# Performance work log

Measured on AMD Instinct MI355X. Metric: run time of the kernel, lower is better.

Reference implementation:

```python
import jax, jax.numpy as jnp
import numpy as np

B, T, V, R = 512, 24, 32000, 32
# Scale keeps both the selected chain (factor ~ sqrt(R)*c per step) and the
# vocab-marginalized chain (factor ~ sqrt(V*R)*c per step) inside fp32 range.
CORE_SCALE = (R * np.sqrt(V)) ** -0.5


def setup_inputs() -> dict:
    key = jax.random.key(0)
    k1, k2, k3, k4 = jax.random.split(key, 4)
    y = jax.random.randint(k1, (B, T), 0, V)                      # (B, T) token ids
    alpha = jax.random.normal(k2, (1, R), dtype=jnp.float32)      # left boundary
    beta = jax.random.normal(k3, (1, R), dtype=jnp.float32)       # right boundary
    core = jax.random.normal(k4, (1, R, V, R), dtype=jnp.float32) * CORE_SCALE
    return {"y": y, "alpha": alpha, "beta": beta, "core": core}


def _mps_fwd(alpha, beta, core, y):
    a = alpha[0]                                   # (R,)
    b = beta[0]                                    # (R,)
    cores = jnp.transpose(core[0], (1, 0, 2))      # (V, R, R): per-token transfer matrices
    bsz, seq = y.shape

    # --- unnormalized p(y): chain of selected R x R matrices (marginalize_mask = 0) ---
    sel = jnp.moveaxis(cores[y], 1, 0)             # (T, B, R, R) gathered transfer matrices
    init = jnp.broadcast_to(a, (bsz, R))           # (B, R)

    def step(state, M):                            # state: (B, R), M: (B, R, R)
        return jnp.einsum('br,brs->bs', state, M), None

    state, _ = jax.lax.scan(step, init, sel)
    p_tilde = state @ b                            # (B,)

    # --- normalization: every position marginalized over vocab (free pos-0 leg also summed) ---
    m = cores.sum(axis=0)                          # (R, R) marginalized transfer matrix

    def zstep(v, _):                               # v: (R,)
        return v @ m, None

    vz, _ = jax.lax.scan(zstep, a, None, length=seq)
    z = (vz @ b) * bsz                             # z_one is identical per row; .sum() over batch

    return jnp.concatenate([p_tilde, z[None]])     # (B + 1,): [p_tilde..., z]


def reference(y, alpha, beta, core):
    return _mps_fwd(alpha, beta, core, y)
```

## Files before the change

### kernel.cpp

```cpp
#include <hip/hip_runtime.h>

#define RNK 32
#define VOC 32000
#define BSZ 512
#define SEQ 24

#define CHAIN_BLOCKS 512
#define RED_CHUNKS 125
#define REDUCE_BLOCKS (32 * RED_CHUNKS)
#define DEPTH 6

typedef const __attribute__((address_space(1))) void* as1_cvp;
typedef __attribute__((address_space(3))) void* as3_vp;

__device__ __forceinline__ void issue_matrix_load(const float* src_tok,
                                                  float* lds_base, int lane) {
    const int r  = lane >> 3;
    const int c0 = (lane & 7) * 4;
    #pragma unroll
    for (int j = 0; j < 4; ++j) {
        const float* src = src_tok + (size_t)(j * 8 + r) * ((size_t)VOC * RNK) + c0;
        __builtin_amdgcn_global_load_lds((as1_cvp)src, (as3_vp)(lds_base + j * 256), 16, 0, 0);
    }
}

__global__ __launch_bounds__(64) void fused_kernel(const float* __restrict__ core,
                                                   const int* __restrict__ y,
                                                   const float* __restrict__ alpha,
                                                   const float* __restrict__ beta,
                                                   float* __restrict__ out,
                                                   float* __restrict__ gm) {
    __shared__ float mbuf[DEPTH * 1024];

    const int tid = threadIdx.x;

    if (blockIdx.x < CHAIN_BLOCKS) {
        const int lane = tid;
        const int s    = lane & 31;
        const int half = lane >> 5;
        const int row  = blockIdx.x;

        int   ytok  = (lane < SEQ) ? y[row * SEQ + lane] : 0;
        float state = alpha[s];
        float betav = beta[s];

        asm volatile("s_waitcnt vmcnt(0)" ::: "memory");

        #pragma unroll
        for (int pt = 0; pt < DEPTH; ++pt) {
            const int tok = __shfl(ytok, pt, 64);
            issue_matrix_load(core + (size_t)tok * RNK, mbuf + pt * 1024, lane);
        }

        #pragma unroll
        for (int t = 0; t < SEQ; ++t) {
            if      (t <= SEQ - 6) asm volatile("s_waitcnt vmcnt(20)" ::: "memory");
            else if (t == SEQ - 5) asm volatile("s_waitcnt vmcnt(16)" ::: "memory");
            else if (t == SEQ - 4) asm volatile("s_waitcnt vmcnt(12)" ::: "memory");
            else if (t == SEQ - 3) asm volatile("s_waitcnt vmcnt(8)"  ::: "memory");
            else if (t == SEQ - 2) asm volatile("s_waitcnt vmcnt(4)"  ::: "memory");
            else                   asm volatile("s_waitcnt vmcnt(0)"  ::: "memory");
            __builtin_amdgcn_sched_barrier(0);

            if (t + DEPTH < SEQ) {
                const int tok = __shfl(ytok, t + DEPTH, 64);
                issue_matrix_load(core + (size_t)tok * RNK,
                                  mbuf + ((t + DEPTH) % DEPTH) * 1024, lane);
            }

            const float* M = mbuf + (t % DEPTH) * 1024;
            float a0 = 0.f, a1 = 0.f, a2 = 0.f, a3 = 0.f;
            #pragma unroll
            for (int i = 0; i < 16; i += 4) {
                a0 = fmaf(__shfl(state, half * 16 + i + 0, 64), M[(half * 16 + i + 0) * 32 + s], a0);
                a1 = fmaf(__shfl(state, half * 16 + i + 1, 64), M[(half * 16 + i + 1) * 32 + s], a1);
                a2 = fmaf(__shfl(state, half * 16 + i + 2, 64), M[(half * 16 + i + 2) * 32 + s], a2);
                a3 = fmaf(__shfl(state, half * 16 + i + 3, 64), M[(half * 16 + i + 3) * 32 + s], a3);
            }
            const float acc = (a0 + a1) + (a2 + a3);
            state = acc + __shfl_xor(acc, 32, 64);
        }

        float p = state * betav;
        #pragma unroll
        for (int m = 16; m >= 1; m >>= 1) p += __shfl_xor(p, m, 64);
        if (lane == 0) out[row] = p;
    } else {
        const int bid   = blockIdx.x - CHAIN_BLOCKS;
        const int r     = bid & 31;
        const int chunk = bid >> 5;

        const float4* slab = (const float4*)(core + (size_t)r * VOC * RNK);
        const int base = chunk * 2048 + tid;

        float a0 = 0.f, a1 = 0.f, a2 = 0.f, a3 = 0.f;
        #pragma unroll
        for (int i = 0; i < 32; ++i) {
            float4 v = slab[base + i * 64];
            a0 += v.x; a1 += v.y; a2 += v.z; a3 += v.w;
        }

        #pragma unroll
        for (int mask = 8; mask <= 32; mask <<= 1) {
            a0 += __shfl_xor(a0, mask, 64);
            a1 += __shfl_xor(a1, mask, 64);
            a2 += __shfl_xor(a2, mask, 64);
            a3 += __shfl_xor(a3, mask, 64);
        }
        if (tid < 8) {
            const int s0 = tid * 4;
            atomicAdd(&gm[r * RNK + s0 + 0], a0);
            atomicAdd(&gm[r * RNK + s0 + 1], a1);
            atomicAdd(&gm[r * RNK + s0 + 2], a2);
            atomicAdd(&gm[r * RNK + s0 + 3], a3);
        }
    }
}

__global__ void zchain_kernel(const float* __restrict__ gm,
                              const float* __restrict__ alpha,
                              const float* __restrict__ beta,
                              float* __restrict__ out) {
    const int lane = threadIdx.x & 63;
    const int s    = lane & 31;
    const int half = lane >> 5;

    float col[16];
    #pragma unroll
    for (int i = 0; i < 16; ++i) col[i] = gm[(half * 16 + i) * RNK + s];

    float v = alpha[s];
    #pragma unroll
    for (int t = 0; t < SEQ; ++t) {
        float a0 = 0.f, a1 = 0.f, a2 = 0.f, a3 = 0.f;
        #pragma unroll
        for (int i = 0; i < 16; i += 4) {
            a0 = fmaf(__shfl(v, half * 16 + i + 0, 64), col[i + 0], a0);
            a1 = fmaf(__shfl(v, half * 16 + i + 1, 64), col[i + 1], a1);
            a2 = fmaf(__shfl(v, half * 16 + i + 2, 64), col[i + 2], a2);
            a3 = fmaf(__shfl(v, half * 16 + i + 3, 64), col[i + 3], a3);
        }
        const float acc = (a0 + a1) + (a2 + a3);
        v = acc + __shfl_xor(acc, 32, 64);
    }
    float z = v * beta[s];
    #pragma unroll
    for (int m = 16; m >= 1; m >>= 1) z += __shfl_xor(z, m, 64);
    if (lane == 0) out[BSZ] = z * (float)BSZ;
}

extern "C" void kernel_launch(void* const* d_in, const int* in_sizes, int n_in,
                              void* d_out, int out_size, void* d_ws, size_t ws_size,
                              hipStream_t stream) {
    const int*   y     = (const int*)d_in[0];
    const float* alpha = (const float*)d_in[1];
    const float* beta  = (const float*)d_in[2];
    const float* core  = (const float*)d_in[3];
    float* out = (float*)d_out;
    float* gm  = (float*)d_ws;

    hipMemsetAsync(gm, 0, RNK * RNK * sizeof(float), stream);
    fused_kernel<<<CHAIN_BLOCKS + REDUCE_BLOCKS, 64, 0, stream>>>(core, y, alpha, beta, out, gm);
    zchain_kernel<<<1, 64, 0, stream>>>(gm, alpha, beta, out);
}
```

Measured before the change: 45.64 us.

## Split vocab reduction into its own kernel and fuse z-chain into chain kernel

The vocab-marginalization reduction moves into a standalone 256-thread kernel with fewer loads per thread. The z-chain is folded into the batch chain kernel as one extra block, which removes a separate launch. The chain prefetch pipeline is reworked to use 4-deep prefetch over 5 LDS slots, with the next load issued after the compute. In exchange, the chain blocks no longer run concurrently with the reduction, because the two phases are now serialized across launches.

```diff
diff --git a/kernel.cpp b/kernel.cpp
--- a/kernel.cpp
+++ b/kernel.cpp
@@ -5,10 +5,11 @@
 #define BSZ 512
 #define SEQ 24
 
-#define CHAIN_BLOCKS 512
-#define RED_CHUNKS 125
-#define REDUCE_BLOCKS (32 * RED_CHUNKS)
-#define DEPTH 6
+#define RED_BLOCKS 4000
+#define RED_THREADS 256
+
+#define DEPTH 4
+#define NSLOT 5
 
 typedef const __attribute__((address_space(1))) void* as1_cvp;
 typedef __attribute__((address_space(3))) void* as3_vp;
@@ -24,17 +25,49 @@
     }
 }
 
-__global__ __launch_bounds__(64) void fused_kernel(const float* __restrict__ core,
-                                                   const int* __restrict__ y,
-                                                   const float* __restrict__ alpha,
-                                                   const float* __restrict__ beta,
-                                                   float* __restrict__ out,
-                                                   float* __restrict__ gm) {
-    __shared__ float mbuf[DEPTH * 1024];
+__global__ __launch_bounds__(RED_THREADS) void reduce_kernel(const float* __restrict__ core,
+                                                             float* __restrict__ gm) {
+    const int bid   = blockIdx.x;
+    const int r     = bid & 31;
+    const int chunk = bid >> 5;
+    const int tid   = threadIdx.x;
 
+    const float4* slab = (const float4*)(core + (size_t)r * VOC * RNK);
+    const int base = chunk * 2048 + tid;
+
+    float a0 = 0.f, a1 = 0.f, a2 = 0.f, a3 = 0.f;
+    #pragma unroll
+    for (int i = 0; i < 8; ++i) {
+        float4 v = slab[base + i * 256];
+        a0 += v.x; a1 += v.y; a2 += v.z; a3 += v.w;
+    }
+
+    #pragma unroll
+    for (int mask = 8; mask <= 32; mask <<= 1) {
+        a0 += __shfl_xor(a0, mask, 64);
+        a1 += __shfl_xor(a1, mask, 64);
+        a2 += __shfl_xor(a2, mask, 64);
+        a3 += __shfl_xor(a3, mask, 64);
+    }
+    if ((tid & 63) < 8) {
+        const int s0 = (tid & 7) * 4;
+        atomicAdd(&gm[r * RNK + s0 + 0], a0);
+        atomicAdd(&gm[r * RNK + s0 + 1], a1);
+        atomicAdd(&gm[r * RNK + s0 + 2], a2);
+        atomicAdd(&gm[r * RNK + s0 + 3], a3);
+    }
+}
+
+__global__ __launch_bounds__(64) void chainz_kernel(const float* __restrict__ core,
+                                                    const int* __restrict__ y,
+                                                    const float* __restrict__ alpha,
+                                                    const float* __restrict__ beta,
+                                                    float* __restrict__ out,
+                                                    const float* __restrict__ gm) {
+    __shared__ float mbuf[NSLOT * 1024];
     const int tid = threadIdx.x;
 
-    if (blockIdx.x < CHAIN_BLOCKS) {
+    if (blockIdx.x < BSZ) {
         const int lane = tid;
         const int s    = lane & 31;
         const int half = lane >> 5;
@@ -54,21 +87,13 @@
 
         #pragma unroll
         for (int t = 0; t < SEQ; ++t) {
-            if      (t <= SEQ - 6) asm volatile("s_waitcnt vmcnt(20)" ::: "memory");
-            else if (t == SEQ - 5) asm volatile("s_waitcnt vmcnt(16)" ::: "memory");
-            else if (t == SEQ - 4) asm volatile("s_waitcnt vmcnt(12)" ::: "memory");
+            if      (t <= SEQ - 4) asm volatile("s_waitcnt vmcnt(12)" ::: "memory");
             else if (t == SEQ - 3) asm volatile("s_waitcnt vmcnt(8)"  ::: "memory");
             else if (t == SEQ - 2) asm volatile("s_waitcnt vmcnt(4)"  ::: "memory");
             else                   asm volatile("s_waitcnt vmcnt(0)"  ::: "memory");
             __builtin_amdgcn_sched_barrier(0);
 
-            if (t + DEPTH < SEQ) {
-                const int tok = __shfl(ytok, t + DEPTH, 64);
-                issue_matrix_load(core + (size_t)tok * RNK,
-                                  mbuf + ((t + DEPTH) % DEPTH) * 1024, lane);
-            }
-
-            const float* M = mbuf + (t % DEPTH) * 1024;
+            const float* M = mbuf + (t % NSLOT) * 1024;
             float a0 = 0.f, a1 = 0.f, a2 = 0.f, a3 = 0.f;
             #pragma unroll
             for (int i = 0; i < 16; i += 4) {
@@ -79,6 +104,12 @@
             }
             const float acc = (a0 + a1) + (a2 + a3);
             state = acc + __shfl_xor(acc, 32, 64);
+
+            if (t + DEPTH < SEQ) {
+                const int tok = __shfl(ytok, t + DEPTH, 64);
+                issue_matrix_load(core + (size_t)tok * RNK,
+                                  mbuf + ((t + DEPTH) % NSLOT) * 1024, lane);
+            }
         }
 
         float p = state * betav;
@@ -86,67 +117,32 @@
         for (int m = 16; m >= 1; m >>= 1) p += __shfl_xor(p, m, 64);
         if (lane == 0) out[row] = p;
     } else {
-        const int bid   = blockIdx.x - CHAIN_BLOCKS;
-        const int r     = bid & 31;
-        const int chunk = bid >> 5;
+        const int s    = tid & 31;
+        const int half = tid >> 5;
 
-        const float4* slab = (const float4*)(core + (size_t)r * VOC * RNK);
-        const int base = chunk * 2048 + tid;
+        float col[16];
+        #pragma unroll
+        for (int i = 0; i < 16; ++i) col[i] = gm[(half * 16 + i) * RNK + s];
 
-        float a0 = 0.f, a1 = 0.f, a2 = 0.f, a3 = 0.f;
+        float v = alpha[s];
         #pragma unroll
-        for (int i = 0; i < 32; ++i) {
-            float4 v = slab[base + i * 64];
-            a0 += v.x; a1 += v.y; a2 += v.z; a3 += v.w;
+        for (int t = 0; t < SEQ; ++t) {
+            float a0 = 0.f, a1 = 0.f, a2 = 0.f, a3 = 0.f;
+            #pragma unroll
+            for (int i = 0; i < 16; i += 4) {
+                a0 = fmaf(__shfl(v, half * 16 + i + 0, 64), col[i + 0], a0);
+                a1 = fmaf(__shfl(v, half * 16 + i + 1, 64), col[i + 1], a1);
+                a2 = fmaf(__shfl(v, half * 16 + i + 2, 64), col[i + 2], a2);
+                a3 = fmaf(__shfl(v, half * 16 + i + 3, 64), col[i + 3], a3);
+            }
+            const float acc = (a0 + a1) + (a2 + a3);
+            v = acc + __shfl_xor(acc, 32, 64);
         }
-
+        float z = v * beta[s];
         #pragma unroll
-        for (int mask = 8; mask <= 32; mask <<= 1) {
-            a0 += __shfl_xor(a0, mask, 64);
-            a1 += __shfl_xor(a1, mask, 64);
-            a2 += __shfl_xor(a2, mask, 64);
-            a3 += __shfl_xor(a3, mask, 64);
-        }
-        if (tid < 8) {
-            const int s0 = tid * 4;
-            atomicAdd(&gm[r * RNK + s0 + 0], a0);
-            atomicAdd(&gm[r * RNK + s0 + 1], a1);
-            atomicAdd(&gm[r * RNK + s0 + 2], a2);
-            atomicAdd(&gm[r * RNK + s0 + 3], a3);
-        }
+        for (int m = 16; m >= 1; m >>= 1) z += __shfl_xor(z, m, 64);
+        if (tid == 0) out[BSZ] = z * (float)BSZ;
     }
-}
-
-__global__ void zchain_kernel(const float* __restrict__ gm,
-                              const float* __restrict__ alpha,
-                              const float* __restrict__ beta,
-                              float* __restrict__ out) {
-    const int lane = threadIdx.x & 63;
-    const int s    = lane & 31;
-    const int half = lane >> 5;
-
-    float col[16];
-    #pragma unroll
-    for (int i = 0; i < 16; ++i) col[i] = gm[(half * 16 + i) * RNK + s];
-
-    float v = alpha[s];
-    #pragma unroll
-    for (int t = 0; t < SEQ; ++t) {
-        float a0 = 0.f, a1 = 0.f, a2 = 0.f, a3 = 0.f;
-        #pragma unroll
-        for (int i = 0; i < 16; i += 4) {
-            a0 = fmaf(__shfl(v, half * 16 + i + 0, 64), col[i + 0], a0);
-            a1 = fmaf(__shfl(v, half * 16 + i + 1, 64), col[i + 1], a1);
-            a2 = fmaf(__shfl(v, half * 16 + i + 2, 64), col[i + 2], a2);
-            a3 = fmaf(__shfl(v, half * 16 + i + 3, 64), col[i + 3], a3);
-        }
-        const float acc = (a0 + a1) + (a2 + a3);
-        v = acc + __shfl_xor(acc, 32, 64);
-    }
-    float z = v * beta[s];
-    #pragma unroll
-    for (int m = 16; m >= 1; m >>= 1) z += __shfl_xor(z, m, 64);
-    if (lane == 0) out[BSZ] = z * (float)BSZ;
 }
 
 extern "C" void kernel_launch(void* const* d_in, const int* in_sizes, int n_in,
@@ -160,6 +156,6 @@
     float* gm  = (float*)d_ws;
 
     hipMemsetAsync(gm, 0, RNK * RNK * sizeof(float), stream);
-    fused_kernel<<<CHAIN_BLOCKS + REDUCE_BLOCKS, 64, 0, stream>>>(core, y, alpha, beta, out, gm);
-    zchain_kernel<<<1, 64, 0, stream>>>(gm, alpha, beta, out);
+    reduce_kernel<<<RED_BLOCKS, RED_THREADS, 0, stream>>>(core, gm);
+    chainz_kernel<<<BSZ + 1, 64, 0, stream>>>(core, y, alpha, beta, out, gm);
 }
```

Measured after the change: 75.59 us. 1.66x slower.

## Split selected-matrix chain into left and right halves meeting in the middle

Applied to the files above, without the earlier changes.

Each batch row's 24-step chain becomes two 12-step chains. One block carries alpha forward through the first half and another carries beta backward through the second half, with the right blocks reading transposed matrices. A follow-up kernel takes the dot product of the two state vectors per row and also runs the normalization chain. LDS loads are XOR-swizzled to avoid bank conflicts, and the prefetch now issues after the compute with 5 slots. This halves the serial latency per block and doubles the chain block count, at the cost of a workspace round trip for the state vectors.

```diff
diff --git a/kernel.cpp b/kernel.cpp
--- a/kernel.cpp
+++ b/kernel.cpp
@@ -4,22 +4,25 @@
 #define VOC 32000
 #define BSZ 512
 #define SEQ 24
+#define HSEQ 12
 
-#define CHAIN_BLOCKS 512
+#define LEFT_BLOCKS  BSZ
+#define CHAIN_BLOCKS (2 * BSZ)
 #define RED_CHUNKS 125
 #define REDUCE_BLOCKS (32 * RED_CHUNKS)
-#define DEPTH 6
+#define DEPTH 4
+#define NSLOT 5
 
 typedef const __attribute__((address_space(1))) void* as1_cvp;
 typedef __attribute__((address_space(3))) void* as3_vp;
 
 __device__ __forceinline__ void issue_matrix_load(const float* src_tok,
                                                   float* lds_base, int lane) {
-    const int r  = lane >> 3;
-    const int c0 = (lane & 7) * 4;
+    const int rlo = lane >> 3;
+    const int cq  = ((lane & 7) ^ rlo) * 4;
     #pragma unroll
     for (int j = 0; j < 4; ++j) {
-        const float* src = src_tok + (size_t)(j * 8 + r) * ((size_t)VOC * RNK) + c0;
+        const float* src = src_tok + (size_t)(j * 8 + rlo) * ((size_t)VOC * RNK) + cq;
         __builtin_amdgcn_global_load_lds((as1_cvp)src, (as3_vp)(lds_base + j * 256), 16, 0, 0);
     }
 }
@@ -28,21 +31,37 @@
                                                    const int* __restrict__ y,
                                                    const float* __restrict__ alpha,
                                                    const float* __restrict__ beta,
-                                                   float* __restrict__ out,
+                                                   float* __restrict__ Lv,
+                                                   float* __restrict__ Rv,
                                                    float* __restrict__ gm) {
-    __shared__ float mbuf[DEPTH * 1024];
-
+    __shared__ float mbuf[NSLOT * 1024];
     const int tid = threadIdx.x;
 
     if (blockIdx.x < CHAIN_BLOCKS) {
-        const int lane = tid;
-        const int s    = lane & 31;
-        const int half = lane >> 5;
-        const int row  = blockIdx.x;
+        const bool right = blockIdx.x >= LEFT_BLOCKS;
+        const int  row   = blockIdx.x - (right ? LEFT_BLOCKS : 0);
+        const int  lane  = tid;
+        const int  s     = lane & 31;
+        const int  half  = lane >> 5;
 
-        int   ytok  = (lane < SEQ) ? y[row * SEQ + lane] : 0;
-        float state = alpha[s];
-        float betav = beta[s];
+        int ytok = 0;
+        if (lane < HSEQ) ytok = y[row * SEQ + (right ? (SEQ - 1 - lane) : lane)];
+
+        float state = right ? beta[s] : alpha[s];
+
+        int la[16];
+        if (!right) {
+            #pragma unroll
+            for (int i = 0; i < 16; ++i) {
+                const int r = half * 16 + i;
+                la[i] = r * 32 + ((((s >> 2) ^ (r & 7)) ) << 2) + (s & 3);
+            }
+        } else {
+            #pragma unroll
+            for (int i = 0; i < 16; ++i) {
+                la[i] = s * 32 + ((((half * 4 + (i >> 2)) ^ (s & 7))) << 2) + (i & 3);
+            }
+        }
 
         asm volatile("s_waitcnt vmcnt(0)" ::: "memory");
 
@@ -53,38 +72,33 @@
         }
 
         #pragma unroll
-        for (int t = 0; t < SEQ; ++t) {
-            if      (t <= SEQ - 6) asm volatile("s_waitcnt vmcnt(20)" ::: "memory");
-            else if (t == SEQ - 5) asm volatile("s_waitcnt vmcnt(16)" ::: "memory");
-            else if (t == SEQ - 4) asm volatile("s_waitcnt vmcnt(12)" ::: "memory");
-            else if (t == SEQ - 3) asm volatile("s_waitcnt vmcnt(8)"  ::: "memory");
-            else if (t == SEQ - 2) asm volatile("s_waitcnt vmcnt(4)"  ::: "memory");
-            else                   asm volatile("s_waitcnt vmcnt(0)"  ::: "memory");
+        for (int t = 0; t < HSEQ; ++t) {
+            if      (t <= HSEQ - 4) asm volatile("s_waitcnt vmcnt(12)" ::: "memory");
+            else if (t == HSEQ - 3) asm volatile("s_waitcnt vmcnt(8)"  ::: "memory");
+            else if (t == HSEQ - 2) asm volatile("s_waitcnt vmcnt(4)"  ::: "memory");
+            else                    asm volatile("s_waitcnt vmcnt(0)"  ::: "memory");
             __builtin_amdgcn_sched_barrier(0);
 
-            if (t + DEPTH < SEQ) {
-                const int tok = __shfl(ytok, t + DEPTH, 64);
-                issue_matrix_load(core + (size_t)tok * RNK,
-                                  mbuf + ((t + DEPTH) % DEPTH) * 1024, lane);
-            }
-
-            const float* M = mbuf + (t % DEPTH) * 1024;
+            const float* M = mbuf + (t % NSLOT) * 1024;
             float a0 = 0.f, a1 = 0.f, a2 = 0.f, a3 = 0.f;
             #pragma unroll
             for (int i = 0; i < 16; i += 4) {
-                a0 = fmaf(__shfl(state, half * 16 + i + 0, 64), M[(half * 16 + i + 0) * 32 + s], a0);
-                a1 = fmaf(__shfl(state, half * 16 + i + 1, 64), M[(half * 16 + i + 1) * 32 + s], a1);
-                a2 = fmaf(__shfl(state, half * 16 + i + 2, 64), M[(half * 16 + i + 2) * 32 + s], a2);
-                a3 = fmaf(__shfl(state, half * 16 + i + 3, 64), M[(half * 16 + i + 3) * 32 + s], a3);
+                a0 = fmaf(__shfl(state, half * 16 + i + 0, 64), M[la[i + 0]], a0);
+                a1 = fmaf(__shfl(state, half * 16 + i + 1, 64), M[la[i + 1]], a1);
+                a2 = fmaf(__shfl(state, half * 16 + i + 2, 64), M[la[i + 2]], a2);
+                a3 = fmaf(__shfl(state, half * 16 + i + 3, 64), M[la[i + 3]], a3);
             }
             const float acc = (a0 + a1) + (a2 + a3);
             state = acc + __shfl_xor(acc, 32, 64);
+
+            if (t + DEPTH < HSEQ) {
+                const int tok = __shfl(ytok, t + DEPTH, 64);
+                issue_matrix_load(core + (size_t)tok * RNK,
+                                  mbuf + ((t + DEPTH) % NSLOT) * 1024, lane);
+            }
         }
 
-        float p = state * betav;
-        #pragma unroll
-        for (int m = 16; m >= 1; m >>= 1) p += __shfl_xor(p, m, 64);
-        if (lane == 0) out[row] = p;
+        if (lane < 32) (right ? Rv : Lv)[row * RNK + lane] = state;
     } else {
         const int bid   = blockIdx.x - CHAIN_BLOCKS;
         const int r     = bid & 31;
@@ -117,36 +131,44 @@
     }
 }
 
-__global__ void zchain_kernel(const float* __restrict__ gm,
-                              const float* __restrict__ alpha,
-                              const float* __restrict__ beta,
-                              float* __restrict__ out) {
-    const int lane = threadIdx.x & 63;
-    const int s    = lane & 31;
-    const int half = lane >> 5;
-
-    float col[16];
-    #pragma unroll
-    for (int i = 0; i < 16; ++i) col[i] = gm[(half * 16 + i) * RNK + s];
-
-    float v = alpha[s];
-    #pragma unroll
-    for (int t = 0; t < SEQ; ++t) {
-        float a0 = 0.f, a1 = 0.f, a2 = 0.f, a3 = 0.f;
+__global__ __launch_bounds__(256) void dotz_kernel(const float* __restrict__ Lv,
+                                                   const float* __restrict__ Rv,
+                                                   const float* __restrict__ gm,
+                                                   const float* __restrict__ alpha,
+                                                   const float* __restrict__ beta,
+                                                   float* __restrict__ out) {
+    if (blockIdx.x < 64) {
+        const int row = blockIdx.x * 8 + (threadIdx.x >> 5);
+        const int l   = threadIdx.x & 31;
+        float v = Lv[row * RNK + l] * Rv[row * RNK + l];
         #pragma unroll
-        for (int i = 0; i < 16; i += 4) {
-            a0 = fmaf(__shfl(v, half * 16 + i + 0, 64), col[i + 0], a0);
-            a1 = fmaf(__shfl(v, half * 16 + i + 1, 64), col[i + 1], a1);
-            a2 = fmaf(__shfl(v, half * 16 + i + 2, 64), col[i + 2], a2);
-            a3 = fmaf(__shfl(v, half * 16 + i + 3, 64), col[i + 3], a3);
+        for (int m = 16; m >= 1; m >>= 1) v += __shfl_xor(v, m, 64);
+        if (l == 0) out[row] = v;
+    } else if (threadIdx.x < 64) {
+        const int s    = threadIdx.x & 31;
+        const int half = threadIdx.x >> 5;
+        float col[16];
+        #pragma unroll
+        for (int i = 0; i < 16; ++i) col[i] = gm[(half * 16 + i) * RNK + s];
+        float v = alpha[s];
+        #pragma unroll
+        for (int t = 0; t < SEQ; ++t) {
+            float a0 = 0.f, a1 = 0.f, a2 = 0.f, a3 = 0.f;
+            #pragma unroll
+            for (int i = 0; i < 16; i += 4) {
+                a0 = fmaf(__shfl(v, half * 16 + i + 0, 64), col[i + 0], a0);
+                a1 = fmaf(__shfl(v, half * 16 + i + 1, 64), col[i + 1], a1);
+                a2 = fmaf(__shfl(v, half * 16 + i + 2, 64), col[i + 2], a2);
+                a3 = fmaf(__shfl(v, half * 16 + i + 3, 64), col[i + 3], a3);
+            }
+            const float acc = (a0 + a1) + (a2 + a3);
+            v = acc + __shfl_xor(acc, 32, 64);
         }
-        const float acc = (a0 + a1) + (a2 + a3);
-        v = acc + __shfl_xor(acc, 32, 64);
+        float z = v * beta[s];
+        #pragma unroll
+        for (int m = 16; m >= 1; m >>= 1) z += __shfl_xor(z, m, 64);
+        if (threadIdx.x == 0) out[BSZ] = z * (float)BSZ;
     }
-    float z = v * beta[s];
-    #pragma unroll
-    for (int m = 16; m >= 1; m >>= 1) z += __shfl_xor(z, m, 64);
-    if (lane == 0) out[BSZ] = z * (float)BSZ;
 }
 
 extern "C" void kernel_launch(void* const* d_in, const int* in_sizes, int n_in,
@@ -158,8 +180,11 @@
     const float* core  = (const float*)d_in[3];
     float* out = (float*)d_out;
     float* gm  = (float*)d_ws;
+    float* Lv  = gm + RNK * RNK;
+    float* Rv  = Lv + BSZ * RNK;
 
     hipMemsetAsync(gm, 0, RNK * RNK * sizeof(float), stream);
-    fused_kernel<<<CHAIN_BLOCKS + REDUCE_BLOCKS, 64, 0, stream>>>(core, y, alpha, beta, out, gm);
-    zchain_kernel<<<1, 64, 0, stream>>>(gm, alpha, beta, out);
+    fused_kernel<<<CHAIN_BLOCKS + REDUCE_BLOCKS, 64, 0, stream>>>(
+        core, y, alpha, beta, Lv, Rv, gm);
+    dotz_kernel<<<65, 256, 0, stream>>>(Lv, Rv, gm, alpha, beta, out);
 }
```

Result: no change. 45.27 us (-0.8%).
